# Optimization experiments

Hardware: AMD Instinct MI355X
Metric: run time of the kernel (lower is better)

The kernel has to match this reference:

```python
import jax, jax.numpy as jnp
import numpy as np

B, T, D, H = 64, 512, 128, 256


def _ilin(v, l, u, W):
    # interval-bounded linear with point weight W [O, I]: split pos/neg parts
    Wp = jnp.maximum(W, 0.0)
    Wn = jnp.minimum(W, 0.0)
    return (v @ W.T, l @ Wp.T + u @ Wn.T, u @ Wp.T + l @ Wn.T)


def _imul(a, b):
    # interval * interval: 4 cross-terms, stacked min/max (mirrors `mul` in source)
    av, al, au = a
    bv, bl, bu = b
    cands = jnp.stack([al * bl, al * bu, au * bl, au * bu])
    return (av * bv, cands.min(axis=0), cands.max(axis=0))


def _iadd(a, b):
    return tuple(x + y for x, y in zip(a, b))


def _iact(f, a):
    # monotone elementwise activation applied to val/lb/ub (mirrors `activation`)
    return (f(a[0]), f(a[1]), f(a[2]))


def setup_inputs() -> dict:
    key = jax.random.key(0)
    k0, k1, k2, k3, k4 = jax.random.split(key, 5)
    x_val = jax.random.normal(k0, (B, T, D), jnp.float32)
    eps = 0.05 * jax.random.uniform(k1, (B, T, D), jnp.float32)
    x_lb = x_val - eps
    x_ub = x_val + eps
    s = 1.0 / np.sqrt(H).astype(np.float32)
    W_ih = jax.random.uniform(k2, (4 * H, D), jnp.float32, -s, s)
    W_hh = jax.random.uniform(k3, (4 * H, H), jnp.float32, -s, s)
    b = jax.random.uniform(k4, (4 * H,), jnp.float32, -s, s)
    return {"x_val": x_val, "x_lb": x_lb, "x_ub": x_ub, "W_ih": W_ih, "W_hh": W_hh, "b": b}


def reference(x_val, x_lb, x_ub, W_ih, W_hh, b):
    Hh = W_hh.shape[1]

    def step(carry, xt):
        h, c = carry  # each a (val, lb, ub) triple of [B, H]
        px = _ilin(xt[0], xt[1], xt[2], W_ih)
        ph = _ilin(h[0], h[1], h[2], W_hh)
        pre = tuple(a + bb + b for a, bb in zip(px, ph))  # [B, 4H] triple
        gates = [tuple(t[..., k * Hh:(k + 1) * Hh] for t in pre) for k in range(4)]
        i_g = _iact(jax.nn.sigmoid, gates[0])
        f_g = _iact(jax.nn.sigmoid, gates[1])
        g_g = _iact(jnp.tanh, gates[2])
        o_g = _iact(jax.nn.sigmoid, gates[3])
        c_new = _iadd(_imul(f_g, c), _imul(i_g, g_g))
        h_new = _imul(o_g, _iact(jnp.tanh, c_new))
        return (h_new, c_new), h_new

    Bn = x_val.shape[0]
    z = jnp.zeros((Bn, Hh), x_val.dtype)
    init = ((z, z, z), (z, z, z))
    xs = (x_val.transpose(1, 0, 2), x_lb.transpose(1, 0, 2), x_ub.transpose(1, 0, 2))
    _, hs = jax.lax.scan(step, init, xs)
    # hs: triple of [T, B, H] -> stack as [3, B, T, H] (val, lb, ub)
    return jnp.stack([h.transpose(1, 0, 2) for h in hs], axis=0)
```

## Files before the change

kernel.cpp:

```cpp
#include <hip/hip_runtime.h>
#include <hip/hip_fp16.h>

#define NB 64
#define NT 512
#define ND 128
#define NH 256
#define G4 1024
#define NBT (NB*NT)
#define CSTRIDE ((size_t)NBT * G4)
#define OSTRIDE ((size_t)NBT * NH)

typedef _Float16 f16x2 __attribute__((ext_vector_type(2)));

__device__ __forceinline__ float fdot2u(unsigned a, unsigned b, float c) {
  return __builtin_amdgcn_fdot2(__builtin_bit_cast(f16x2, a),
                                __builtin_bit_cast(f16x2, b), c, false);
}

__device__ __forceinline__ void accV(uint4 w, uint4 hv, float& av) {
  av = fdot2u(w.x, hv.x, av);
  av = fdot2u(w.y, hv.y, av);
  av = fdot2u(w.z, hv.z, av);
  av = fdot2u(w.w, hv.w, av);
}
__device__ __forceinline__ void accMR(uint4 w, uint4 hm, uint4 hr, float& am, float& ar) {
  const unsigned M = 0x7FFF7FFFu;
  am = fdot2u(w.x, hm.x, am); ar = fdot2u(w.x & M, hr.x, ar);
  am = fdot2u(w.y, hm.y, am); ar = fdot2u(w.y & M, hr.y, ar);
  am = fdot2u(w.z, hm.z, am); ar = fdot2u(w.z & M, hr.z, ar);
  am = fdot2u(w.w, hm.w, am); ar = fdot2u(w.w & M, hr.w, ar);
}

__device__ __forceinline__ float qsum4(float x) {
  int v = __builtin_amdgcn_update_dpp(0, __builtin_bit_cast(int, x), 0xB1, 0xF, 0xF, true);
  x += __builtin_bit_cast(float, v);
  v = __builtin_amdgcn_update_dpp(0, __builtin_bit_cast(int, x), 0x4E, 0xF, 0xF, true);
  x += __builtin_bit_cast(float, v);
  return x;
}
__device__ __forceinline__ float sel4(float x0, float x1, float x2, float x3, int q) {
  float a = (q & 1) ? x1 : x0;
  float b = (q & 1) ? x3 : x2;
  return (q & 2) ? b : a;
}

__device__ __forceinline__ float rcpf(float x) { return __builtin_amdgcn_rcpf(x); }
__device__ __forceinline__ float gact(float x, bool is_tanh) {
  float s = is_tanh ? -2.0f : -1.0f;
  float e = __expf(s * x);
  float r = rcpf(1.0f + e);
  return is_tanh ? fmaf(2.0f, r, -1.0f) : r;
}
__device__ __forceinline__ float tanh_f(float x) {
  return fmaf(2.0f, rcpf(1.0f + __expf(-2.0f * x)), -1.0f);
}
__device__ __forceinline__ float min4c(float a, float b, float c, float d) {
  return fminf(fminf(fminf(a, b), c), d);
}
__device__ __forceinline__ float max4c(float a, float b, float c, float d) {
  return fmaxf(fmaxf(fmaxf(a, b), c), d);
}

__global__ void conv_w_kernel(const float* __restrict__ Whh, const float* __restrict__ Wih,
                              uint4* __restrict__ P4, uint4* __restrict__ PIH) {
  int o = blockIdx.x * 256 + threadIdx.x;
  union { uint4 u; __half h[8]; } p;
  if (o < 32768) {
    int t = o & 1023, rc = o >> 10, r = rc >> 3, c8 = rc & 7;
    int j = ((t >> 2) << 2) + r, k = ((t & 3) << 6) + c8 * 8;
    const float* s = Whh + j * NH + k;
#pragma unroll
    for (int i = 0; i < 8; ++i) p.h[i] = __float2half(s[i]);
    P4[o] = p.u;
  } else if (o < 49152) {
    int o3 = o - 32768;
    int t = o3 & 511, rc = o3 >> 9, c = rc >> 3, r = rc & 7;
    int j = ((t >> 2) << 3) + r, k = ((t & 3) << 5) + c * 8;
    const float* s = Wih + j * ND + k;
#pragma unroll
    for (int i = 0; i < 8; ++i) p.h[i] = __float2half(s[i]);
    PIH[o3] = p.u;
  }
}

__global__ __launch_bounds__(512, 2)
void px_kernel(const float* __restrict__ xv, const float* __restrict__ xl,
               const float* __restrict__ xu, const uint4* __restrict__ PIH,
               const float* __restrict__ bias, __half* __restrict__ px) {
  __shared__ __align__(16) __half sv[32 * ND];
  __shared__ __align__(16) __half sm[32 * ND];
  __shared__ __align__(16) __half sr[32 * ND];
  const int t = threadIdx.x;
  const int q = t & 3;
  const int r0 = blockIdx.x * 32;
  const float b0 = bias[2 * t];
  const float b1 = bias[2 * t + 1];
  uint4 w[4][8];
#pragma unroll
  for (int c = 0; c < 4; ++c)
#pragma unroll
    for (int r = 0; r < 8; ++r)
      w[c][r] = PIH[((c * 8 + r) << 9) + t];
  {
    const float4* v4 = (const float4*)(xv + (size_t)r0 * ND);
    const float4* l4 = (const float4*)(xl + (size_t)r0 * ND);
    const float4* u4 = (const float4*)(xu + (size_t)r0 * ND);
    __half2* sv2 = (__half2*)sv; __half2* sm2 = (__half2*)sm; __half2* sr2 = (__half2*)sr;
    for (int i = t; i < 1024; i += 512) {
      float4 v = v4[i], l = l4[i], u = u4[i];
      sv2[2*i]   = __floats2half2_rn(v.x, v.y);
      sv2[2*i+1] = __floats2half2_rn(v.z, v.w);
      sm2[2*i]   = __floats2half2_rn(0.5f*(l.x+u.x), 0.5f*(l.y+u.y));
      sm2[2*i+1] = __floats2half2_rn(0.5f*(l.z+u.z), 0.5f*(l.w+u.w));
      sr2[2*i]   = __floats2half2_rn(0.5f*(u.x-l.x), 0.5f*(u.y-l.y));
      sr2[2*i+1] = __floats2half2_rn(0.5f*(u.z-l.z), 0.5f*(u.w-l.w));
    }
  }
  __syncthreads();
  const uint4* bv = (const uint4*)sv;
  const uint4* bm = (const uint4*)sm;
  const uint4* br = (const uint4*)sr;
  __half2* pxV = (__half2*)px;
  __half2* pxI = (__half2*)(px + CSTRIDE);
  for (int rr = 0; rr < 32; ++rr) {
    uint4 hv[4], hm[4], hr[4];
    const int base = rr * 16 + q * 4;
#pragma unroll
    for (int i = 0; i < 4; ++i) { hv[i] = bv[base+i]; hm[i] = bm[base+i]; hr[i] = br[base+i]; }
    float A[8][3];
#pragma unroll
    for (int r = 0; r < 8; ++r) { A[r][0] = 0.f; A[r][1] = 0.f; A[r][2] = 0.f; }
#pragma unroll
    for (int c = 0; c < 4; ++c)
#pragma unroll
      for (int r = 0; r < 8; ++r) {
        accV(w[c][r], hv[c], A[r][0]);
        accMR(w[c][r], hm[c], hr[c], A[r][1], A[r][2]);
      }
#pragma unroll
    for (int r = 0; r < 8; ++r) {
      A[r][0] = qsum4(A[r][0]); A[r][1] = qsum4(A[r][1]); A[r][2] = qsum4(A[r][2]);
    }
    float v0 = sel4(A[0][0], A[2][0], A[4][0], A[6][0], q) + b0;
    float m0 = sel4(A[0][1], A[2][1], A[4][1], A[6][1], q) + b0;
    float d0 = sel4(A[0][2], A[2][2], A[4][2], A[6][2], q);
    float v1 = sel4(A[1][0], A[3][0], A[5][0], A[7][0], q) + b1;
    float m1 = sel4(A[1][1], A[3][1], A[5][1], A[7][1], q) + b1;
    float d1 = sel4(A[1][2], A[3][2], A[5][2], A[7][2], q);
    size_t ob = (size_t)(r0 + rr) * G4;
    pxV[(ob >> 1) + t] = __floats2half2_rn(v0, v1);
    union { uint2 u; __half2 h[2]; } pi;
    pi.h[0] = __floats2half2_rn(m0 - d0, m0 + d0);
    pi.h[1] = __floats2half2_rn(m1 - d1, m1 + d1);
    *(uint2*)(pxI + ob + 2 * t) = pi.u;
  }
}

__global__ __launch_bounds__(1024, 4)
void lstm_kernel(const uint4* __restrict__ P4, const __half* __restrict__ px,
                 float* __restrict__ out) {
  __shared__ uint4 sLW[8192];
  __shared__ __align__(16) __half sH[2][4][72];
  __shared__ __align__(16) float sG[2][G4];
  float2* sGp = (float2*)sG;
  const int t = threadIdx.x;
  const bool intv = blockIdx.x >= NB;
  const int b = intv ? blockIdx.x - NB : blockIdx.x;
  const int q = t & 3;
  uint4 Wp[3][8];
#pragma unroll
  for (int r = 0; r < 3; ++r)
#pragma unroll
    for (int c8 = 0; c8 < 8; ++c8)
      Wp[r][c8] = P4[((r * 8 + c8) << 10) + t];
#pragma unroll
  for (int r = 0; r < 3; ++r)
#pragma unroll
    for (int c8 = 0; c8 < 8; ++c8)
      asm volatile("" : "+v"(Wp[r][c8].x), "+v"(Wp[r][c8].y),
                        "+v"(Wp[r][c8].z), "+v"(Wp[r][c8].w));
#pragma unroll
  for (int c8 = 0; c8 < 8; ++c8)
    sLW[(c8 << 10) + t] = P4[((24 + c8) << 10) + t];
  const bool is_tanh = ((t >> 8) == 2);
  if (t < 288) ((unsigned*)sH)[t] = 0u;
  __syncthreads();
  float* outb = out + (size_t)b * NT * NH;

  if (!intv) {
    const __half* pxb = px + (size_t)b * NT * G4;
    float cv = 0.f, hv_p = 0.f;
    float pv = __half2float(pxb[t]);
    for (int ts = 0; ts < NT; ++ts) {
      if (ts > 0 && t < NH) outb[(size_t)(ts - 1) * NH + t] = hv_p;
      const int tsn = (ts + 1 < NT) ? ts + 1 : ts;
      float nv = __half2float(pxb[(size_t)tsn * G4 + t]);
      float A0 = 0.f, A1 = 0.f, A2 = 0.f, A3 = 0.f;
#pragma unroll
      for (int c8 = 0; c8 < 8; ++c8) {
        uint4 wl3 = sLW[(c8 << 10) + t];
        uint4 hv = *(const uint4*)(&sH[0][q][c8 * 8]);
        accV(Wp[0][c8], hv, A0);
        accV(Wp[1][c8], hv, A1);
        accV(Wp[2][c8], hv, A2);
        accV(wl3, hv, A3);
      }
      A0 = qsum4(A0); A1 = qsum4(A1); A2 = qsum4(A2); A3 = qsum4(A3);
      float av = sel4(A0, A1, A2, A3, q);
      float gt = gact(pv + av, is_tanh);
      sG[0][t] = gt;
      __syncthreads();
      if (t < NH) {
        float iv = sG[0][t], fv = sG[0][NH + t], gv = sG[0][2 * NH + t], ov = sG[0][3 * NH + t];
        cv = fmaf(fv, cv, iv * gv);
        float hvn = ov * tanh_f(cv);
        hv_p = hvn;
        sH[0][t >> 6][t & 63] = __float2half(hvn);
      }
      __syncthreads();
      pv = nv;
    }
    if (t < NH) outb[(size_t)(NT - 1) * NH + t] = hv_p;
  } else {
    const __half2* pI = (const __half2*)(px + CSTRIDE) + (size_t)b * NT * G4;
    float cl = 0.f, cu = 0.f, hl_p = 0.f, hu_p = 0.f;
    __half2 plu = pI[t];
    for (int ts = 0; ts < NT; ++ts) {
      if (ts > 0 && t < NH) {
        size_t o = (size_t)(ts - 1) * NH + t;
        outb[OSTRIDE + o] = hl_p; outb[2 * OSTRIDE + o] = hu_p;
      }
      const int tsn = (ts + 1 < NT) ? ts + 1 : ts;
      __half2 nlu = pI[(size_t)tsn * G4 + t];
      float M0 = 0.f, M1 = 0.f, M2 = 0.f, M3 = 0.f;
      float R0 = 0.f, R1 = 0.f, R2 = 0.f, R3 = 0.f;
#pragma unroll
      for (int c8 = 0; c8 < 8; ++c8) {
        uint4 wl3 = sLW[(c8 << 10) + t];
        uint4 hm = *(const uint4*)(&sH[0][q][c8 * 8]);
        uint4 hr = *(const uint4*)(&sH[1][q][c8 * 8]);
        accMR(Wp[0][c8], hm, hr, M0, R0);
        accMR(Wp[1][c8], hm, hr, M1, R1);
        accMR(Wp[2][c8], hm, hr, M2, R2);
        accMR(wl3, hm, hr, M3, R3);
      }
      M0 = qsum4(M0); M1 = qsum4(M1); M2 = qsum4(M2); M3 = qsum4(M3);
      R0 = qsum4(R0); R1 = qsum4(R1); R2 = qsum4(R2); R3 = qsum4(R3);
      float m = sel4(M0, M1, M2, M3, q);
      float d = sel4(R0, R1, R2, R3, q);
      float pl = __low2float(plu), pu = __high2float(plu);
      float gl = gact(pl + (m - d), is_tanh);
      float gu = gact(pu + (m + d), is_tanh);
      sGp[t] = make_float2(gl, gu);
      __syncthreads();
      if (t < NH) {
        float2 gi = sGp[t], gf = sGp[NH + t], gg = sGp[2 * NH + t], go = sGp[3 * NH + t];
        float il = gi.x, iu = gi.y, fl = gf.x, fu = gf.y;
        float gl_ = gg.x, gu_ = gg.y, ol = go.x, ou = go.y;
        float p0 = fl*cl, p1 = fl*cu, p2 = fu*cl, p3 = fu*cu;
        float fcl = min4c(p0, p1, p2, p3);
        float fcu = max4c(p0, p1, p2, p3);
        p0 = il*gl_; p1 = il*gu_; p2 = iu*gl_; p3 = iu*gu_;
        float igl = min4c(p0, p1, p2, p3);
        float igu = max4c(p0, p1, p2, p3);
        cl = fcl + igl; cu = fcu + igu;
        float tl = tanh_f(cl), tu = tanh_f(cu);
        p0 = ol*tl; p1 = ol*tu; p2 = ou*tl; p3 = ou*tu;
        float hl = min4c(p0, p1, p2, p3);
        float hu = max4c(p0, p1, p2, p3);
        hl_p = hl; hu_p = hu;
        sH[0][t >> 6][t & 63] = __float2half(0.5f * (hl + hu));
        sH[1][t >> 6][t & 63] = __float2half(0.5f * (hu - hl));
      }
      __syncthreads();
      plu = nlu;
    }
    if (t < NH) {
      size_t o = (size_t)(NT - 1) * NH + t;
      outb[OSTRIDE + o] = hl_p; outb[2 * OSTRIDE + o] = hu_p;
    }
  }
}

extern "C" void kernel_launch(void* const* d_in, const int* in_sizes, int n_in,
                              void* d_out, int out_size, void* d_ws, size_t ws_size,
                              hipStream_t stream) {
  const float* xv   = (const float*)d_in[0];
  const float* xl   = (const float*)d_in[1];
  const float* xu   = (const float*)d_in[2];
  const float* Wih  = (const float*)d_in[3];
  const float* Whh  = (const float*)d_in[4];
  const float* bias = (const float*)d_in[5];
  float* out = (float*)d_out;
  char* ws = (char*)d_ws;
  uint4*  P4  = (uint4*)ws;
  uint4*  PIH = (uint4*)(ws + 512 * 1024);
  __half* px  = (__half*)(ws + 768 * 1024);

  conv_w_kernel<<<192, 256, 0, stream>>>(Whh, Wih, P4, PIH);
  px_kernel<<<NBT / 32, 512, 0, stream>>>(xv, xl, xu, PIH, bias, px);
  lstm_kernel<<<2 * NB, 1024, 0, stream>>>(P4, px, out);
}
```

Before: 2.284 ms.

## Interleave gate rows per quad, combine gates via DPP, double-buffer h

Reorders the packed W_hh/W_ih rows and bias so that the four lanes of each quad hold the i, f, g and o gates of the same hidden unit. The gate values are then exchanged with DPP quad broadcasts, and every thread updates the cell state redundantly. This removes the shared-memory gate buffer and one of the two block barriers per timestep. The hidden state is double-buffered in LDS so a single barrier per step is enough, and output stores are spread across quad lanes. The cost is redundant elementwise math on all 1024 threads and a changed weight layout.

```diff
diff --git a/kernel.cpp b/kernel.cpp
--- a/kernel.cpp
+++ b/kernel.cpp
@@ -43,6 +43,11 @@
   float b = (q & 1) ? x3 : x2;
   return (q & 2) ? b : a;
 }
+template <int PAT>
+__device__ __forceinline__ float qb(float x) {
+  return __builtin_bit_cast(float,
+      __builtin_amdgcn_update_dpp(0, __builtin_bit_cast(int, x), PAT, 0xF, 0xF, true));
+}
 
 __device__ __forceinline__ float rcpf(float x) { return __builtin_amdgcn_rcpf(x); }
 __device__ __forceinline__ float gact(float x, bool is_tanh) {
@@ -66,8 +71,8 @@
   int o = blockIdx.x * 256 + threadIdx.x;
   union { uint4 u; __half h[8]; } p;
   if (o < 32768) {
-    int t = o & 1023, rc = o >> 10, r = rc >> 3, c8 = rc & 7;
-    int j = ((t >> 2) << 2) + r, k = ((t & 3) << 6) + c8 * 8;
+    int t = o & 1023, rc = o >> 10, g = rc >> 3, c8 = rc & 7;
+    int j = (g << 8) + (t >> 2), k = ((t & 3) << 6) + c8 * 8;
     const float* s = Whh + j * NH + k;
 #pragma unroll
     for (int i = 0; i < 8; ++i) p.h[i] = __float2half(s[i]);
@@ -75,7 +80,8 @@
   } else if (o < 49152) {
     int o3 = o - 32768;
     int t = o3 & 511, rc = o3 >> 9, c = rc >> 3, r = rc & 7;
-    int j = ((t >> 2) << 3) + r, k = ((t & 3) << 5) + c * 8;
+    int j = ((r & 3) << 8) + ((t >> 2) << 1) + (r >> 2);
+    int k = ((t & 3) << 5) + c * 8;
     const float* s = Wih + j * ND + k;
 #pragma unroll
     for (int i = 0; i < 8; ++i) p.h[i] = __float2half(s[i]);
@@ -93,8 +99,9 @@
   const int t = threadIdx.x;
   const int q = t & 3;
   const int r0 = blockIdx.x * 32;
-  const float b0 = bias[2 * t];
-  const float b1 = bias[2 * t + 1];
+  const int jb = ((t & 1) << 9) + (t >> 1);
+  const float b0 = bias[jb];
+  const float b1 = bias[jb + 256];
   uint4 w[4][8];
 #pragma unroll
   for (int c = 0; c < 4; ++c)
@@ -160,76 +167,67 @@
 void lstm_kernel(const uint4* __restrict__ P4, const __half* __restrict__ px,
                  float* __restrict__ out) {
   __shared__ uint4 sLW[8192];
-  __shared__ __align__(16) __half sH[2][4][72];
-  __shared__ __align__(16) float sG[2][G4];
-  float2* sGp = (float2*)sG;
+  __shared__ __align__(16) __half sH[2][2][4][72];
   const int t = threadIdx.x;
   const bool intv = blockIdx.x >= NB;
   const int b = intv ? blockIdx.x - NB : blockIdx.x;
   const int q = t & 3;
+  const int n = t >> 2;
   uint4 Wp[3][8];
 #pragma unroll
-  for (int r = 0; r < 3; ++r)
+  for (int g = 0; g < 3; ++g)
 #pragma unroll
     for (int c8 = 0; c8 < 8; ++c8)
-      Wp[r][c8] = P4[((r * 8 + c8) << 10) + t];
-#pragma unroll
-  for (int r = 0; r < 3; ++r)
+      Wp[g][c8] = P4[((g * 8 + c8) << 10) + t];
+#pragma unroll
+  for (int g = 0; g < 3; ++g)
 #pragma unroll
     for (int c8 = 0; c8 < 8; ++c8)
-      asm volatile("" : "+v"(Wp[r][c8].x), "+v"(Wp[r][c8].y),
-                        "+v"(Wp[r][c8].z), "+v"(Wp[r][c8].w));
+      asm volatile("" : "+v"(Wp[g][c8].x), "+v"(Wp[g][c8].y),
+                        "+v"(Wp[g][c8].z), "+v"(Wp[g][c8].w));
 #pragma unroll
   for (int c8 = 0; c8 < 8; ++c8)
     sLW[(c8 << 10) + t] = P4[((24 + c8) << 10) + t];
-  const bool is_tanh = ((t >> 8) == 2);
-  if (t < 288) ((unsigned*)sH)[t] = 0u;
+  const bool is_tanh = (q == 2);
+  if (t < 576) ((unsigned*)sH)[t] = 0u;
   __syncthreads();
   float* outb = out + (size_t)b * NT * NH;
+  int buf = 0;
 
   if (!intv) {
     const __half* pxb = px + (size_t)b * NT * G4;
-    float cv = 0.f, hv_p = 0.f;
+    float cv = 0.f;
     float pv = __half2float(pxb[t]);
     for (int ts = 0; ts < NT; ++ts) {
-      if (ts > 0 && t < NH) outb[(size_t)(ts - 1) * NH + t] = hv_p;
       const int tsn = (ts + 1 < NT) ? ts + 1 : ts;
       float nv = __half2float(pxb[(size_t)tsn * G4 + t]);
       float A0 = 0.f, A1 = 0.f, A2 = 0.f, A3 = 0.f;
 #pragma unroll
       for (int c8 = 0; c8 < 8; ++c8) {
         uint4 wl3 = sLW[(c8 << 10) + t];
-        uint4 hv = *(const uint4*)(&sH[0][q][c8 * 8]);
+        uint4 hv = *(const uint4*)(&sH[buf][0][q][c8 * 8]);
         accV(Wp[0][c8], hv, A0);
         accV(Wp[1][c8], hv, A1);
         accV(Wp[2][c8], hv, A2);
         accV(wl3, hv, A3);
       }
       A0 = qsum4(A0); A1 = qsum4(A1); A2 = qsum4(A2); A3 = qsum4(A3);
-      float av = sel4(A0, A1, A2, A3, q);
-      float gt = gact(pv + av, is_tanh);
-      sG[0][t] = gt;
+      float a = sel4(A0, A1, A2, A3, q);
+      float gt = gact(pv + a, is_tanh);
+      float ig = qb<0x00>(gt), fg = qb<0x55>(gt), gg = qb<0xAA>(gt), og = qb<0xFF>(gt);
+      cv = fmaf(fg, cv, ig * gg);
+      float hvn = og * tanh_f(cv);
+      if (q == 1) outb[(size_t)ts * NH + n] = hvn;
+      if (q == 0) sH[buf ^ 1][0][n >> 6][n & 63] = __float2half(hvn);
       __syncthreads();
-      if (t < NH) {
-        float iv = sG[0][t], fv = sG[0][NH + t], gv = sG[0][2 * NH + t], ov = sG[0][3 * NH + t];
-        cv = fmaf(fv, cv, iv * gv);
-        float hvn = ov * tanh_f(cv);
-        hv_p = hvn;
-        sH[0][t >> 6][t & 63] = __float2half(hvn);
-      }
-      __syncthreads();
+      buf ^= 1;
       pv = nv;
     }
-    if (t < NH) outb[(size_t)(NT - 1) * NH + t] = hv_p;
   } else {
     const __half2* pI = (const __half2*)(px + CSTRIDE) + (size_t)b * NT * G4;
-    float cl = 0.f, cu = 0.f, hl_p = 0.f, hu_p = 0.f;
+    float cl = 0.f, cu = 0.f;
     __half2 plu = pI[t];
     for (int ts = 0; ts < NT; ++ts) {
-      if (ts > 0 && t < NH) {
-        size_t o = (size_t)(ts - 1) * NH + t;
-        outb[OSTRIDE + o] = hl_p; outb[2 * OSTRIDE + o] = hu_p;
-      }
       const int tsn = (ts + 1 < NT) ? ts + 1 : ts;
       __half2 nlu = pI[(size_t)tsn * G4 + t];
       float M0 = 0.f, M1 = 0.f, M2 = 0.f, M3 = 0.f;
@@ -237,8 +235,8 @@
 #pragma unroll
       for (int c8 = 0; c8 < 8; ++c8) {
         uint4 wl3 = sLW[(c8 << 10) + t];
-        uint4 hm = *(const uint4*)(&sH[0][q][c8 * 8]);
-        uint4 hr = *(const uint4*)(&sH[1][q][c8 * 8]);
+        uint4 hm = *(const uint4*)(&sH[buf][0][q][c8 * 8]);
+        uint4 hr = *(const uint4*)(&sH[buf][1][q][c8 * 8]);
         accMR(Wp[0][c8], hm, hr, M0, R0);
         accMR(Wp[1][c8], hm, hr, M1, R1);
         accMR(Wp[2][c8], hm, hr, M2, R2);
@@ -251,33 +249,26 @@
       float pl = __low2float(plu), pu = __high2float(plu);
       float gl = gact(pl + (m - d), is_tanh);
       float gu = gact(pu + (m + d), is_tanh);
-      sGp[t] = make_float2(gl, gu);
+      float il = qb<0x00>(gl), fl = qb<0x55>(gl), gl_ = qb<0xAA>(gl), ol = qb<0xFF>(gl);
+      float iu = qb<0x00>(gu), fu = qb<0x55>(gu), gu_ = qb<0xAA>(gu), ou = qb<0xFF>(gu);
+      float p0 = fl * cl, p1 = fl * cu, p2 = fu * cl, p3 = fu * cu;
+      float fcl = min4c(p0, p1, p2, p3);
+      float fcu = max4c(p0, p1, p2, p3);
+      p0 = il * gl_; p1 = il * gu_; p2 = iu * gl_; p3 = iu * gu_;
+      float igl = min4c(p0, p1, p2, p3);
+      float igu = max4c(p0, p1, p2, p3);
+      cl = fcl + igl; cu = fcu + igu;
+      float tl = tanh_f(cl), tu = tanh_f(cu);
+      p0 = ol * tl; p1 = ol * tu; p2 = ou * tl; p3 = ou * tu;
+      float hl = min4c(p0, p1, p2, p3);
+      float hu = max4c(p0, p1, p2, p3);
+      if (q == 2) outb[OSTRIDE + (size_t)ts * NH + n] = hl;
+      if (q == 3) outb[2 * OSTRIDE + (size_t)ts * NH + n] = hu;
+      if (q == 0) sH[buf ^ 1][0][n >> 6][n & 63] = __float2half(0.5f * (hl + hu));
+      if (q == 1) sH[buf ^ 1][1][n >> 6][n & 63] = __float2half(0.5f * (hu - hl));
       __syncthreads();
-      if (t < NH) {
-        float2 gi = sGp[t], gf = sGp[NH + t], gg = sGp[2 * NH + t], go = sGp[3 * NH + t];
-        float il = gi.x, iu = gi.y, fl = gf.x, fu = gf.y;
-        float gl_ = gg.x, gu_ = gg.y, ol = go.x, ou = go.y;
-        float p0 = fl*cl, p1 = fl*cu, p2 = fu*cl, p3 = fu*cu;
-        float fcl = min4c(p0, p1, p2, p3);
-        float fcu = max4c(p0, p1, p2, p3);
-        p0 = il*gl_; p1 = il*gu_; p2 = iu*gl_; p3 = iu*gu_;
-        float igl = min4c(p0, p1, p2, p3);
-        float igu = max4c(p0, p1, p2, p3);
-        cl = fcl + igl; cu = fcu + igu;
-        float tl = tanh_f(cl), tu = tanh_f(cu);
-        p0 = ol*tl; p1 = ol*tu; p2 = ou*tl; p3 = ou*tu;
-        float hl = min4c(p0, p1, p2, p3);
-        float hu = max4c(p0, p1, p2, p3);
-        hl_p = hl; hu_p = hu;
-        sH[0][t >> 6][t & 63] = __float2half(0.5f * (hl + hu));
-        sH[1][t >> 6][t & 63] = __float2half(0.5f * (hu - hl));
-      }
-      __syncthreads();
+      buf ^= 1;
       plu = nlu;
-    }
-    if (t < NH) {
-      size_t o = (size_t)(NT - 1) * NH + t;
-      outb[OSTRIDE + o] = hl_p; outb[2 * OSTRIDE + o] = hu_p;
     }
   }
 }
```

Result: slower. 2.693 ms (+17.9%).

## Compute input projection with MFMA 16x16x16 f16 instead of fdot2

Applied to the files above, without the earlier changes.

Replaces the fdot2-based input-projection kernel with an MFMA version. Each wave computes a 16-row tile across all 1024 gate columns, with the weights repacked into the B-fragment layout, and the interval radius uses |W| via a sign mask. This removes the scalar dot-product and LDS staging cost of the precompute stage. In exchange, the output stores become narrow, scattered half writes per element, and weight fragments are reloaded from global memory on every column tile.

```diff
diff --git a/kernel.cpp b/kernel.cpp
--- a/kernel.cpp
+++ b/kernel.cpp
@@ -11,6 +11,8 @@
 #define OSTRIDE ((size_t)NBT * NH)
 
 typedef _Float16 f16x2 __attribute__((ext_vector_type(2)));
+typedef _Float16 f16x4 __attribute__((ext_vector_type(4)));
+typedef float f32x4 __attribute__((ext_vector_type(4)));
 
 __device__ __forceinline__ float fdot2u(unsigned a, unsigned b, float c) {
   return __builtin_amdgcn_fdot2(__builtin_bit_cast(f16x2, a),
@@ -61,8 +63,13 @@
   return fmaxf(fmaxf(fmaxf(a, b), c), d);
 }
 
+__device__ __forceinline__ f16x4 h4(unsigned a, unsigned b) {
+  uint2 u = make_uint2(a, b);
+  return __builtin_bit_cast(f16x4, u);
+}
+
 __global__ void conv_w_kernel(const float* __restrict__ Whh, const float* __restrict__ Wih,
-                              uint4* __restrict__ P4, uint4* __restrict__ PIH) {
+                              uint4* __restrict__ P4, uint4* __restrict__ PB) {
   int o = blockIdx.x * 256 + threadIdx.x;
   union { uint4 u; __half h[8]; } p;
   if (o < 32768) {
@@ -74,85 +81,81 @@
     P4[o] = p.u;
   } else if (o < 49152) {
     int o3 = o - 32768;
-    int t = o3 & 511, rc = o3 >> 9, c = rc >> 3, r = rc & 7;
-    int j = ((t >> 2) << 3) + r, k = ((t & 3) << 5) + c * 8;
-    const float* s = Wih + j * ND + k;
-#pragma unroll
-    for (int i = 0; i < 8; ++i) p.h[i] = __float2half(s[i]);
-    PIH[o3] = p.u;
+    int l = o3 & 63, rest = o3 >> 6;
+    int kp = rest & 3, nt = rest >> 2;
+    int j = nt * 16 + (l & 15);
+    int k0 = kp * 32 + ((l >> 4) << 2);
+    const float* s = Wih + j * ND + k0;
+#pragma unroll
+    for (int i = 0; i < 4; ++i) { p.h[i] = __float2half(s[i]); p.h[4 + i] = __float2half(s[16 + i]); }
+    PB[o3] = p.u;
   }
 }
 
-__global__ __launch_bounds__(512, 2)
-void px_kernel(const float* __restrict__ xv, const float* __restrict__ xl,
-               const float* __restrict__ xu, const uint4* __restrict__ PIH,
-               const float* __restrict__ bias, __half* __restrict__ px) {
-  __shared__ __align__(16) __half sv[32 * ND];
-  __shared__ __align__(16) __half sm[32 * ND];
-  __shared__ __align__(16) __half sr[32 * ND];
-  const int t = threadIdx.x;
-  const int q = t & 3;
-  const int r0 = blockIdx.x * 32;
-  const float b0 = bias[2 * t];
-  const float b1 = bias[2 * t + 1];
-  uint4 w[4][8];
-#pragma unroll
-  for (int c = 0; c < 4; ++c)
-#pragma unroll
-    for (int r = 0; r < 8; ++r)
-      w[c][r] = PIH[((c * 8 + r) << 9) + t];
+__global__ __launch_bounds__(256, 2)
+void px_mfma(const float* __restrict__ xv, const float* __restrict__ xl,
+             const float* __restrict__ xu, const uint4* __restrict__ PB,
+             const float* __restrict__ bias, __half* __restrict__ px) {
+  const int l = threadIdx.x & 63;
+  const int w = threadIdx.x >> 6;
+  const int rt = blockIdx.x * 64 + w * 16;
+  const int li = l & 15, g = l >> 4;
+  const unsigned M = 0x7FFF7FFFu;
+  f16x4 av[8], am[8], ar[8];
   {
-    const float4* v4 = (const float4*)(xv + (size_t)r0 * ND);
-    const float4* l4 = (const float4*)(xl + (size_t)r0 * ND);
-    const float4* u4 = (const float4*)(xu + (size_t)r0 * ND);
-    __half2* sv2 = (__half2*)sv; __half2* sm2 = (__half2*)sm; __half2* sr2 = (__half2*)sr;
-    for (int i = t; i < 1024; i += 512) {
-      float4 v = v4[i], l = l4[i], u = u4[i];
-      sv2[2*i]   = __floats2half2_rn(v.x, v.y);
-      sv2[2*i+1] = __floats2half2_rn(v.z, v.w);
-      sm2[2*i]   = __floats2half2_rn(0.5f*(l.x+u.x), 0.5f*(l.y+u.y));
-      sm2[2*i+1] = __floats2half2_rn(0.5f*(l.z+u.z), 0.5f*(l.w+u.w));
-      sr2[2*i]   = __floats2half2_rn(0.5f*(u.x-l.x), 0.5f*(u.y-l.y));
-      sr2[2*i+1] = __floats2half2_rn(0.5f*(u.z-l.z), 0.5f*(u.w-l.w));
+    const int row = rt + li;
+    const float* pv = xv + (size_t)row * ND + g * 4;
+    const float* pl = xl + (size_t)row * ND + g * 4;
+    const float* pu = xu + (size_t)row * ND + g * 4;
+#pragma unroll
+    for (int ks = 0; ks < 8; ++ks) {
+      float4 vv = *(const float4*)(pv + ks * 16);
+      float4 ll = *(const float4*)(pl + ks * 16);
+      float4 uu = *(const float4*)(pu + ks * 16);
+      av[ks][0] = (_Float16)vv.x; av[ks][1] = (_Float16)vv.y;
+      av[ks][2] = (_Float16)vv.z; av[ks][3] = (_Float16)vv.w;
+      am[ks][0] = (_Float16)(0.5f * (ll.x + uu.x)); am[ks][1] = (_Float16)(0.5f * (ll.y + uu.y));
+      am[ks][2] = (_Float16)(0.5f * (ll.z + uu.z)); am[ks][3] = (_Float16)(0.5f * (ll.w + uu.w));
+      ar[ks][0] = (_Float16)(0.5f * (uu.x - ll.x)); ar[ks][1] = (_Float16)(0.5f * (uu.y - ll.y));
+      ar[ks][2] = (_Float16)(0.5f * (uu.z - ll.z)); ar[ks][3] = (_Float16)(0.5f * (uu.w - ll.w));
     }
   }
-  __syncthreads();
-  const uint4* bv = (const uint4*)sv;
-  const uint4* bm = (const uint4*)sm;
-  const uint4* br = (const uint4*)sr;
-  __half2* pxV = (__half2*)px;
+  __half*  pxV = px;
   __half2* pxI = (__half2*)(px + CSTRIDE);
-  for (int rr = 0; rr < 32; ++rr) {
-    uint4 hv[4], hm[4], hr[4];
-    const int base = rr * 16 + q * 4;
-#pragma unroll
-    for (int i = 0; i < 4; ++i) { hv[i] = bv[base+i]; hm[i] = bm[base+i]; hr[i] = br[base+i]; }
-    float A[8][3];
-#pragma unroll
-    for (int r = 0; r < 8; ++r) { A[r][0] = 0.f; A[r][1] = 0.f; A[r][2] = 0.f; }
-#pragma unroll
-    for (int c = 0; c < 4; ++c)
-#pragma unroll
-      for (int r = 0; r < 8; ++r) {
-        accV(w[c][r], hv[c], A[r][0]);
-        accMR(w[c][r], hm[c], hr[c], A[r][1], A[r][2]);
-      }
-#pragma unroll
-    for (int r = 0; r < 8; ++r) {
-      A[r][0] = qsum4(A[r][0]); A[r][1] = qsum4(A[r][1]); A[r][2] = qsum4(A[r][2]);
-    }
-    float v0 = sel4(A[0][0], A[2][0], A[4][0], A[6][0], q) + b0;
-    float m0 = sel4(A[0][1], A[2][1], A[4][1], A[6][1], q) + b0;
-    float d0 = sel4(A[0][2], A[2][2], A[4][2], A[6][2], q);
-    float v1 = sel4(A[1][0], A[3][0], A[5][0], A[7][0], q) + b1;
-    float m1 = sel4(A[1][1], A[3][1], A[5][1], A[7][1], q) + b1;
-    float d1 = sel4(A[1][2], A[3][2], A[5][2], A[7][2], q);
-    size_t ob = (size_t)(r0 + rr) * G4;
-    pxV[(ob >> 1) + t] = __floats2half2_rn(v0, v1);
-    union { uint2 u; __half2 h[2]; } pi;
-    pi.h[0] = __floats2half2_rn(m0 - d0, m0 + d0);
-    pi.h[1] = __floats2half2_rn(m1 - d1, m1 + d1);
-    *(uint2*)(pxI + ob + 2 * t) = pi.u;
+  for (int nt = 0; nt < 64; ++nt) {
+    uint4 B0 = PB[(nt * 4 + 0) * 64 + l];
+    uint4 B1 = PB[(nt * 4 + 1) * 64 + l];
+    uint4 B2 = PB[(nt * 4 + 2) * 64 + l];
+    uint4 B3 = PB[(nt * 4 + 3) * 64 + l];
+    f32x4 accv = {0.f, 0.f, 0.f, 0.f};
+    f32x4 accm = {0.f, 0.f, 0.f, 0.f};
+    f32x4 accr = {0.f, 0.f, 0.f, 0.f};
+#pragma unroll
+    for (int kp = 0; kp < 4; ++kp) {
+      uint4 B = (kp == 0) ? B0 : (kp == 1) ? B1 : (kp == 2) ? B2 : B3;
+      f16x4 blo = h4(B.x, B.y);
+      f16x4 bhi = h4(B.z, B.w);
+      f16x4 alo = h4(B.x & M, B.y & M);
+      f16x4 ahi = h4(B.z & M, B.w & M);
+      int k0 = kp * 2, k1 = kp * 2 + 1;
+      accv = __builtin_amdgcn_mfma_f32_16x16x16f16(av[k0], blo, accv, 0, 0, 0);
+      accm = __builtin_amdgcn_mfma_f32_16x16x16f16(am[k0], blo, accm, 0, 0, 0);
+      accr = __builtin_amdgcn_mfma_f32_16x16x16f16(ar[k0], alo, accr, 0, 0, 0);
+      accv = __builtin_amdgcn_mfma_f32_16x16x16f16(av[k1], bhi, accv, 0, 0, 0);
+      accm = __builtin_amdgcn_mfma_f32_16x16x16f16(am[k1], bhi, accm, 0, 0, 0);
+      accr = __builtin_amdgcn_mfma_f32_16x16x16f16(ar[k1], ahi, accr, 0, 0, 0);
+    }
+    const int j = nt * 16 + li;
+    const float bb = bias[j];
+#pragma unroll
+    for (int e = 0; e < 4; ++e) {
+      size_t rr = (size_t)(rt + g * 4 + e);
+      float v = accv[e] + bb;
+      float m = accm[e] + bb;
+      float d = accr[e];
+      pxV[rr * G4 + j] = __float2half(v);
+      pxI[rr * G4 + j] = __floats2half2_rn(m - d, m + d);
+    }
   }
 }
 
@@ -293,11 +296,11 @@
   const float* bias = (const float*)d_in[5];
   float* out = (float*)d_out;
   char* ws = (char*)d_ws;
-  uint4*  P4  = (uint4*)ws;
-  uint4*  PIH = (uint4*)(ws + 512 * 1024);
-  __half* px  = (__half*)(ws + 768 * 1024);
-
-  conv_w_kernel<<<192, 256, 0, stream>>>(Whh, Wih, P4, PIH);
-  px_kernel<<<NBT / 32, 512, 0, stream>>>(xv, xl, xu, PIH, bias, px);
+  uint4*  P4 = (uint4*)ws;
+  uint4*  PB = (uint4*)(ws + 512 * 1024);
+  __half* px = (__half*)(ws + 768 * 1024);
+
+  conv_w_kernel<<<192, 256, 0, stream>>>(Whh, Wih, P4, PB);
+  px_mfma<<<NBT / 64, 256, 0, stream>>>(xv, xl, xu, PB, bias, px);
   lstm_kernel<<<2 * NB, 1024, 0, stream>>>(P4, px, out);
 }
```

New measurement: 2.051 ms (median of 2 runs). -10.2%, faster.
